# Performance work log

Hardware: AMD Instinct MI355X
Metric: run time of the kernel (lower is better)

## Reference

```python
import jax, jax.numpy as jnp
import numpy as np

CHANNEL_DIM = 256
RATE = 4
KSIZE = 2 * RATE - 1  # odd=True


def bilinear_kernel(size, normalize=False):
    factor = (size + 1) // 2
    center = factor - 1 if size % 2 == 1 else factor - 0.5
    og = np.ogrid[:size, :size]
    kern = (1 - abs(og[0] - center) / factor) * (1 - abs(og[1] - center) / factor)
    if normalize:
        kern = kern / kern.sum()
    return kern.astype(np.float32)


def setup_inputs() -> dict:
    key = jax.random.key(0)
    x = jax.random.normal(key, (4, CHANNEL_DIM, 64, 64), dtype=jnp.float32)
    # The torch module builds a [C, C, k, k] weight that is block-diagonal:
    # weight[c, c] = bilinear kernel, all cross-channel blocks are zero.
    # We store only the nonzero diagonal as a depthwise kernel [C, 1, k, k]
    # (OIHW with feature_group_count=C), which computes identical math.
    kern = jnp.asarray(bilinear_kernel(KSIZE, normalize=False))  # [k, k]
    weight = jnp.broadcast_to(kern[None, None], (CHANNEL_DIM, 1, KSIZE, KSIZE))
    return {"x": x, "weight": weight}


def reference(x, weight):
    # F.conv_transpose2d(x, W, stride=r) with no padding/output_padding is
    # equivalent to a cross-correlation of the input dilated by r (lhs_dilation)
    # with the spatially-flipped kernel and padding k-1 on each side.
    # The bilinear kernel is symmetric, so the flip is a no-op.
    k = weight.shape[-1]
    return jax.lax.conv_general_dilated(
        x, weight,
        window_strides=(1, 1),
        padding=((k - 1, k - 1), (k - 1, k - 1)),
        lhs_dilation=(RATE, RATE),
        dimension_numbers=("NCHW", "OIHW", "NCHW"),
        feature_group_count=CHANNEL_DIM,
    )  # -> [N, C, (H-1)*rate + k, (W-1)*rate + k] = [4, 256, 259, 259]
```

## Files before the change

kernel.cpp:

```cpp
#include <hip/hip_runtime.h>


#define IH 64
#define IW 64
#define OH 259
#define OW 259
#define OROW 67081

typedef float float4u __attribute__((ext_vector_type(4), aligned(4)));

__global__ __launch_bounds__(256) void upsample4x_strip(
    const float* __restrict__ x, float* __restrict__ out)
{
    const int lane  = threadIdx.x & 63;
    const int g     = blockIdx.x * 4 + (threadIdx.x >> 6);
    const int strip = g & 7;
    const int nc    = g >> 3;

    const int q0 = strip * 8;
    const int q1 = (strip == 7) ? 65 : q0 + 8;

    const float* __restrict__ xp = x + (size_t)nc * (IH * IW);
    float* __restrict__ ob = out + (size_t)nc * OROW;

    float r[10], rm[10];
#pragma unroll
    for (int i = 0; i < 10; ++i) {
        const int ri = q0 - 1 + i;
        r[i] = (ri >= 0 && ri < IH) ? xp[ri * IW + lane] : 0.0f;
    }
#pragma unroll
    for (int i = 0; i < 10; ++i) {
        rm[i] = __shfl_up(r[i], 1);
        if (lane == 0) rm[i] = 0.0f;
    }

#pragma unroll
    for (int j = 0; j < 9; ++j) {
        const int q = q0 + j;
        if (q < q1) {
            const float xl  = r[j],     xh  = r[j + 1];
            const float xlm = rm[j],    xhm = rm[j + 1];

#pragma unroll
            for (int py = 0; py < 4; ++py) {
                const int oy = 4 * q + py;
                if (oy < OH) {
                    const float wyl = 0.25f * (float)(3 - py);
                    const float wyh = 0.25f * (float)(py + 1);
                    float B = wyl * xl  + wyh * xh;
                    float A = wyl * xlm + wyh * xhm;

                    float e1 = 0.5f * (A + B);
                    float e0 = 0.5f * (A + e1);
                    float e2 = 0.5f * (e1 + B);

                    float* rp = ob + (size_t)oy * OW;
                    float4u v = {e0, e1, e2, B};
                    ((float4u*)rp)[lane] = v;

                    if (lane == 63) {
                        float4u t = {B, 0.75f * B, 0.5f * B, 0.25f * B};
                        *(float4u*)(rp + 255) = t;
                    }
                }
            }
        }
    }
}

extern "C" void kernel_launch(void* const* d_in, const int* in_sizes, int n_in,
                              void* d_out, int out_size, void* d_ws, size_t ws_size,
                              hipStream_t stream)
{
    const float* x = (const float*)d_in[0];
    float* out = (float*)d_out;

    upsample4x_strip<<<2048, 256, 0, stream>>>(x, out);
}
```

Baseline: 294.2 us.

## Realign row stores to 16-byte boundaries via per-row phase-shifted templates

Each output row begins at an offset that is not a multiple of 16 bytes, so the float4 stores were misaligned. The kernel now works out each row's alignment phase from the channel index and row parity, and templates the store on that phase. Each lane then writes an aligned float4 that straddles two input columns, using a down-shuffled neighbour. Edge lanes write the ragged head and tail elements. This adds shuffles, template code paths and some scalar edge stores in exchange for aligned wide stores.

```diff
diff --git a/kernel.cpp b/kernel.cpp
--- a/kernel.cpp
+++ b/kernel.cpp
@@ -8,6 +8,89 @@
 #define OROW 67081
 
 typedef float float4u __attribute__((ext_vector_type(4), aligned(4)));
+typedef float float4a __attribute__((ext_vector_type(4), aligned(16)));
+
+template<int S>
+__device__ __forceinline__ void store_row(float* __restrict__ rp, int lane,
+                                          float A, float B, float C)
+{
+    static_assert(S >= 0 && S <= 3, "bad S");
+    if constexpr (S == 0) {
+        float e1 = 0.5f * (A + B);
+        float4a v = {0.5f * (A + e1), e1, 0.5f * (e1 + B), B};
+        ((float4a*)rp)[lane] = v;
+        if (lane == 63) {
+            float4u t = {B, 0.75f * B, 0.5f * B, 0.25f * B};
+            *(float4u*)(rp + 255) = t;
+        }
+    } else {
+        float e[4];
+#pragma unroll
+        for (int j = 0; j < 4; ++j) {
+            const int px = (j - S) & 3;
+            const float wl = 0.25f * (float)(3 - px);
+            const float wh = 0.25f * (float)(px + 1);
+            e[j] = (j < S) ? (wl * A + wh * B)
+                           : (wl * B + wh * C);
+        }
+        float4a v = {e[0], e[1], e[2], e[3]};
+        *(float4a*)(rp + (4 - S) + 4 * lane) = v;
+        if (lane == 0) {
+#pragma unroll
+            for (int i = 0; i < 4 - S; ++i)
+                rp[i] = 0.25f * (float)(i + 1) * B;
+        }
+        if (lane == 63) {
+            if constexpr (S == 3) rp[257] = 0.5f * B;
+            if constexpr (S >= 2) rp[258] = 0.25f * B;
+        }
+    }
+}
+
+template<int NC3, int PY>
+__device__ __forceinline__ void row_py(float* __restrict__ rp0, int lane,
+                                       float rl, float rh,
+                                       float rul, float ruh,
+                                       float rdl, float rdh)
+{
+    constexpr float wyl = 0.25f * (float)(3 - PY);
+    constexpr float wyh = 0.25f * (float)(PY + 1);
+    const float B = wyl * rl  + wyh * rh;
+    const float A = wyl * rul + wyh * ruh;
+    const float C = wyl * rdl + wyh * rdh;
+    store_row<(NC3 + 3 * PY) & 3>(rp0 + PY * OW, lane, A, B, C);
+}
+
+template<int NC3>
+__device__ __forceinline__ void do_strip(const float* __restrict__ xp,
+                                         float* __restrict__ ob,
+                                         int q0, int q1, int lane)
+{
+    float r[10], ru[10], rd[10];
+#pragma unroll
+    for (int i = 0; i < 10; ++i) {
+        const int ri = q0 - 1 + i;
+        r[i] = (ri >= 0 && ri < IH) ? xp[ri * IW + lane] : 0.0f;
+    }
+#pragma unroll
+    for (int i = 0; i < 10; ++i) {
+        ru[i] = __shfl_up(r[i], 1);   if (lane == 0)  ru[i] = 0.0f;
+        rd[i] = __shfl_down(r[i], 1); if (lane == 63) rd[i] = 0.0f;
+    }
+
+#pragma unroll
+    for (int j = 0; j < 9; ++j) {
+        const int q = q0 + j;
+        if (q < q1) {
+            float* rp0 = ob + (size_t)(4 * q) * OW;
+            row_py<NC3, 0>(rp0, lane, r[j], r[j+1], ru[j], ru[j+1], rd[j], rd[j+1]);
+            row_py<NC3, 1>(rp0, lane, r[j], r[j+1], ru[j], ru[j+1], rd[j], rd[j+1]);
+            row_py<NC3, 2>(rp0, lane, r[j], r[j+1], ru[j], ru[j+1], rd[j], rd[j+1]);
+            if (4 * q + 3 < OH)
+                row_py<NC3, 3>(rp0, lane, r[j], r[j+1], ru[j], ru[j+1], rd[j], rd[j+1]);
+        }
+    }
+}
 
 __global__ __launch_bounds__(256) void upsample4x_strip(
     const float* __restrict__ x, float* __restrict__ out)
@@ -23,49 +106,11 @@
     const float* __restrict__ xp = x + (size_t)nc * (IH * IW);
     float* __restrict__ ob = out + (size_t)nc * OROW;
 
-    float r[10], rm[10];
-#pragma unroll
-    for (int i = 0; i < 10; ++i) {
-        const int ri = q0 - 1 + i;
-        r[i] = (ri >= 0 && ri < IH) ? xp[ri * IW + lane] : 0.0f;
-    }
-#pragma unroll
-    for (int i = 0; i < 10; ++i) {
-        rm[i] = __shfl_up(r[i], 1);
-        if (lane == 0) rm[i] = 0.0f;
-    }
-
-#pragma unroll
-    for (int j = 0; j < 9; ++j) {
-        const int q = q0 + j;
-        if (q < q1) {
-            const float xl  = r[j],     xh  = r[j + 1];
-            const float xlm = rm[j],    xhm = rm[j + 1];
-
-#pragma unroll
-            for (int py = 0; py < 4; ++py) {
-                const int oy = 4 * q + py;
-                if (oy < OH) {
-                    const float wyl = 0.25f * (float)(3 - py);
-                    const float wyh = 0.25f * (float)(py + 1);
-                    float B = wyl * xl  + wyh * xh;
-                    float A = wyl * xlm + wyh * xhm;
-
-                    float e1 = 0.5f * (A + B);
-                    float e0 = 0.5f * (A + e1);
-                    float e2 = 0.5f * (e1 + B);
-
-                    float* rp = ob + (size_t)oy * OW;
-                    float4u v = {e0, e1, e2, B};
-                    ((float4u*)rp)[lane] = v;
-
-                    if (lane == 63) {
-                        float4u t = {B, 0.75f * B, 0.5f * B, 0.25f * B};
-                        *(float4u*)(rp + 255) = t;
-                    }
-                }
-            }
-        }
+    switch (nc & 3) {
+        case 0: do_strip<0>(xp, ob, q0, q1, lane); break;
+        case 1: do_strip<1>(xp, ob, q0, q1, lane); break;
+        case 2: do_strip<2>(xp, ob, q0, q1, lane); break;
+        default: do_strip<3>(xp, ob, q0, q1, lane); break;
     }
 }
 
```

Result: no change. 297.0 us (+1.0%).
